# Kernel optimization log

Hardware: AMD Instinct MI355X
Metric: run time of the kernel (lower is better)

## Reference

```python
import jax, jax.numpy as jnp
import numpy as np

BN_EPS = 1e-5
B, G, IN, OUT = 8192, 430, 25, 4  # batch, num small linears, in/out per linear


def _bn(x, gamma, beta):
    # BatchNorm1d in training mode: biased batch statistics over the batch axis
    m = jnp.mean(x, axis=0)
    v = jnp.var(x, axis=0)
    return (x - m) * jax.lax.rsqrt(v + BN_EPS) * gamma + beta


def setup_inputs() -> dict:
    key = jax.random.key(0)
    ks = jax.random.split(key, 20)

    def lin(k, fan_in, fan_out):
        bound = 1.0 / np.sqrt(fan_in)
        kw, kb = jax.random.split(k)
        W = jax.random.uniform(kw, (fan_in, fan_out), jnp.float32, -bound, bound)
        b = jax.random.uniform(kb, (fan_out,), jnp.float32, -bound, bound)
        return W, b

    X = jax.random.normal(ks[0], (B, G, IN), jnp.float32)
    # 430 small linears as one stacked tensor [G, 25, 4]
    bound = 1.0 / np.sqrt(IN)
    Wg = jax.random.uniform(ks[1], (G, IN, OUT), jnp.float32, -bound, bound)
    bg = jax.random.uniform(ks[2], (G, OUT), jnp.float32, -bound, bound)

    W3, b3 = lin(ks[3], 1720, 1024)
    W4, b4 = lin(ks[4], 1024, 512)
    W5, b5 = lin(ks[5], 512, 256)
    W6, b6 = lin(ks[6], 256, 64)
    W7, b7 = lin(ks[7], 64, 32)
    W8, b8 = lin(ks[8], 32, 2)

    g3, be3 = jnp.ones((1024,), jnp.float32), jnp.zeros((1024,), jnp.float32)
    g4, be4 = jnp.ones((512,), jnp.float32), jnp.zeros((512,), jnp.float32)
    g5, be5 = jnp.ones((256,), jnp.float32), jnp.zeros((256,), jnp.float32)

    return dict(X=X, Wg=Wg, bg=bg, W3=W3, b3=b3, g3=g3, be3=be3,
                W4=W4, b4=b4, g4=g4, be4=be4, W5=W5, b5=b5, g5=g5, be5=be5,
                W6=W6, b6=b6, W7=W7, b7=b7, W8=W8, b8=b8)


def reference(X, Wg, bg, W3, b3, g3, be3, W4, b4, g4, be4,
              W5, b5, g5, be5, W6, b6, W7, b7, W8, b8):
    # Fused batched GEMM replacing the 430-iteration Python loop + cats:
    # [B,G,25] x [G,25,4] -> [B,G,4] -> [B,1720]
    h = jnp.einsum('bgi,gio->bgo', X, Wg) + bg
    h = h.reshape(X.shape[0], -1)  # [B, 1720]
    # Dropout layers are identity (deterministic reference); BN uses batch stats
    h = _bn(h @ W3 + b3, g3, be3)
    h = _bn(h @ W4 + b4, g4, be4)
    h = _bn(h @ W5 + b5, g5, be5)
    h = h @ W6 + b6
    h = h @ W7 + b7
    return h @ W8 + b8  # [B, 2]
```

## Files before the change

### kernel.cpp

```cpp
#include <hip/hip_runtime.h>


typedef __attribute__((ext_vector_type(8))) short bfrag;
typedef __attribute__((ext_vector_type(4))) float f32x4v;

__device__ __forceinline__ float4 ld4(const float* p) {
    return *reinterpret_cast<const float4*>(p);
}
__device__ __forceinline__ void st4(float* p, float4 v) {
    *reinterpret_cast<float4*>(p) = v;
}
__device__ __forceinline__ unsigned short f2b(float f) {
    union { float f; unsigned u; } v; v.f = f;
    unsigned r = v.u + 0x7fffu + ((v.u >> 16) & 1u);
    return (unsigned short)(r >> 16);
}
__device__ __forceinline__ float b2f(unsigned short b) {
    union { unsigned u; float f; } v; v.u = (unsigned)b << 16;
    return v.f;
}
__device__ __forceinline__ void async16(unsigned short* lds,
                                        const unsigned short* g) {
    __builtin_amdgcn_global_load_lds(
        (const __attribute__((address_space(1))) void*)g,
        (__attribute__((address_space(3))) void*)lds, 16, 0, 0);
}

__global__ __launch_bounds__(256) void k_grouped(
    const float* __restrict__ X, const float* __restrict__ Wg,
    const float* __restrict__ bg, unsigned short* __restrict__ H0)
{
    __shared__ float Xs[6400];
    const int tid = threadIdx.x;
    const size_t base = (size_t)blockIdx.x * 6400;
    #pragma unroll
    for (int c = 0; c < 25; ++c)
        Xs[c * 256 + tid] = X[base + c * 256 + tid];
    __syncthreads();

    const int idx = blockIdx.x * 256 + tid;
    const int b = idx / 430;
    const int g = idx - b * 430;
    const float* __restrict__ w = Wg + g * 100;
    float4 acc = ld4(bg + g * 4);
    const float* x = &Xs[tid * 25];
    #pragma unroll
    for (int i = 0; i < 25; ++i) {
        const float xi = x[i];
        const float4 wv = ld4(w + i * 4);
        acc.x = fmaf(xi, wv.x, acc.x);
        acc.y = fmaf(xi, wv.y, acc.y);
        acc.z = fmaf(xi, wv.z, acc.z);
        acc.w = fmaf(xi, wv.w, acc.w);
    }
    ushort4 o;
    o.x = f2b(acc.x); o.y = f2b(acc.y); o.z = f2b(acc.z); o.w = f2b(acc.w);
    unsigned short* row = H0 + (size_t)b * 1728;
    *reinterpret_cast<ushort4*>(row + g * 4) = o;
    if (g == 429) {
        const ushort4 z = {0, 0, 0, 0};
        *reinterpret_cast<ushort4*>(row + 1720) = z;
        *reinterpret_cast<ushort4*>(row + 1724) = z;
    }
}

__global__ __launch_bounds__(256) void k_transpose_w(
    const float* __restrict__ W, unsigned short* __restrict__ Wt,
    int K, int N, int Kpad)
{
    __shared__ float t[32][33];
    const int tx = threadIdx.x, ty = threadIdx.y;
    const int k0 = blockIdx.y * 32, n0 = blockIdx.x * 32;
    #pragma unroll
    for (int r = 0; r < 4; ++r) {
        const int k = k0 + ty + r * 8;
        t[ty + r * 8][tx] = (k < K) ? W[(size_t)k * N + n0 + tx] : 0.f;
    }
    __syncthreads();
    #pragma unroll
    for (int r = 0; r < 4; ++r) {
        const int n = n0 + ty + r * 8;
        Wt[(size_t)n * Kpad + k0 + tx] = f2b(t[tx][ty + r * 8]);
    }
}

__global__ __launch_bounds__(256) void k_scale_w(
    const float* __restrict__ W,
    const float* __restrict__ affa, const float* __restrict__ affc,
    unsigned short* __restrict__ Wt, float* __restrict__ bpart,
    int K, int N)
{
    __shared__ float t[32][33];
    __shared__ float red[8][33];
    const int tx = threadIdx.x, ty = threadIdx.y;
    const int k0 = blockIdx.y * 32, n0 = blockIdx.x * 32;
    #pragma unroll
    for (int r = 0; r < 4; ++r)
        t[ty + r * 8][tx] = W[(size_t)(k0 + ty + r * 8) * N + n0 + tx];
    __syncthreads();
    #pragma unroll
    for (int r = 0; r < 4; ++r) {
        const int n = n0 + ty + r * 8;
        Wt[(size_t)n * K + k0 + tx] = f2b(affa[k0 + tx] * t[tx][ty + r * 8]);
    }
    float s = 0.f;
    #pragma unroll
    for (int j = 0; j < 4; ++j) {
        const int kl = ty * 4 + j;
        s = fmaf(affc[k0 + kl], t[kl][tx], s);
    }
    red[ty][tx] = s;
    __syncthreads();
    if (ty == 0) {
        float acc = red[0][tx];
        #pragma unroll
        for (int r = 1; r < 8; ++r) acc += red[r][tx];
        bpart[(size_t)blockIdx.y * N + n0 + tx] = acc;
    }
}

template<bool BPART>
__global__ __launch_bounds__(256) void k_gemm(
    const unsigned short* __restrict__ A,
    const unsigned short* __restrict__ Bt,
    const float* __restrict__ bias,
    const float* __restrict__ bpart, int nbp,
    unsigned short* __restrict__ Y, float* __restrict__ partial,
    int M, int N, int Ka)
{
    __shared__ __align__(16) unsigned short As[128 * 64];
    __shared__ __align__(16) unsigned short Bs[128 * 64];

    const int tid = threadIdx.x;
    const int m0 = blockIdx.y * 128, n0 = blockIdx.x * 128;
    const int lane = tid & 63, wid = tid >> 6;
    const int wm = wid >> 1, wn = wid & 1;
    const int lr = lane & 15, hi = lane >> 4;

    const int srow = wid * 32 + (lane >> 3);
    const int scol = (lane & 7) * 8;
    const unsigned short* Ap = A + (size_t)(m0 + srow) * Ka + scol;
    const unsigned short* Bp = Bt + (size_t)(n0 + srow) * Ka + scol;
    unsigned short* Asd = &As[(wid * 32) * 64];
    unsigned short* Bsd = &Bs[(wid * 32) * 64];

    f32x4v acc[4][4] = {};

    const int Ksteps = Ka >> 6;
    #pragma unroll
    for (int c = 0; c < 4; ++c) {
        async16(Asd + c * 8 * 64, Ap + (size_t)(c * 8) * Ka);
        async16(Bsd + c * 8 * 64, Bp + (size_t)(c * 8) * Ka);
    }

    for (int s = 0; s < Ksteps; ++s) {
        __syncthreads();
        #pragma unroll
        for (int kc = 0; kc < 64; kc += 32) {
            bfrag af[4], bf[4];
            #pragma unroll
            for (int mt = 0; mt < 4; ++mt)
                af[mt] = *reinterpret_cast<const bfrag*>(
                    &As[(wm * 64 + mt * 16 + lr) * 64 + kc + hi * 8]);
            #pragma unroll
            for (int nt = 0; nt < 4; ++nt)
                bf[nt] = *reinterpret_cast<const bfrag*>(
                    &Bs[(wn * 64 + nt * 16 + lr) * 64 + kc + hi * 8]);
            #pragma unroll
            for (int mt = 0; mt < 4; ++mt)
                #pragma unroll
                for (int nt = 0; nt < 4; ++nt)
                    acc[mt][nt] = __builtin_amdgcn_mfma_f32_16x16x32_bf16(
                        af[mt], bf[nt], acc[mt][nt], 0, 0, 0);
        }
        __syncthreads();
        if (s + 1 < Ksteps) {
            const int k0 = (s + 1) << 6;
            #pragma unroll
            for (int c = 0; c < 4; ++c) {
                async16(Asd + c * 8 * 64, Ap + (size_t)(c * 8) * Ka + k0);
                async16(Bsd + c * 8 * 64, Bp + (size_t)(c * 8) * Ka + k0);
            }
        }
    }

    float bcol[4];
    #pragma unroll
    for (int nt = 0; nt < 4; ++nt) {
        const int n = n0 + wn * 64 + nt * 16 + lr;
        float b = bias[n];
        if (BPART)
            for (int t = 0; t < nbp; ++t) b += bpart[(size_t)t * N + n];
        bcol[nt] = b;
    }

    float csum[4] = {0.f, 0.f, 0.f, 0.f}, csq[4] = {0.f, 0.f, 0.f, 0.f};
    #pragma unroll
    for (int mt = 0; mt < 4; ++mt)
        #pragma unroll
        for (int e = 0; e < 4; ++e) {
            const int m = m0 + wm * 64 + mt * 16 + hi * 4 + e;
            #pragma unroll
            for (int nt = 0; nt < 4; ++nt) {
                const float v = acc[mt][nt][e] + bcol[nt];
                Y[(size_t)m * N + n0 + wn * 64 + nt * 16 + lr] = f2b(v);
                csum[nt] += v; csq[nt] += v * v;
            }
        }

    __syncthreads();
    float* redS = (float*)As;
    float* redQ = (float*)Bs;
    const int slot = wm * 4 + hi;
    #pragma unroll
    for (int nt = 0; nt < 4; ++nt) {
        const int c = wn * 64 + nt * 16 + lr;
        redS[slot * 128 + c] = csum[nt];
        redQ[slot * 128 + c] = csq[nt];
    }
    __syncthreads();
    if (tid < 128) {
        float s = 0.f, q = 0.f;
        #pragma unroll
        for (int t = 0; t < 8; ++t) {
            s += redS[t * 128 + tid];
            q += redQ[t * 128 + tid];
        }
        partial[(size_t)blockIdx.y * (2 * N) + n0 + tid] = s;
        partial[(size_t)blockIdx.y * (2 * N) + N + n0 + tid] = q;
    }
}

__global__ __launch_bounds__(256) void k_bn_finalize(
    const float* __restrict__ partial,
    const float* __restrict__ gamma, const float* __restrict__ beta,
    float* __restrict__ affa, float* __restrict__ affc,
    int N, int Mtiles, float invB)
{
    const int c = blockIdx.x * 256 + threadIdx.x;
    if (c >= N) return;
    float S = 0.f, Q = 0.f;
    for (int t = 0; t < Mtiles; ++t) {
        S += partial[(size_t)t * 2 * N + c];
        Q += partial[(size_t)t * 2 * N + N + c];
    }
    const float mean = S * invB;
    const float var = fmaxf(Q * invB - mean * mean, 0.f);
    const float s = rsqrtf(var + 1e-5f);
    const float a = gamma[c] * s;
    affa[c] = a;
    affc[c] = beta[c] - mean * a;
}

__global__ __launch_bounds__(256) void k_tail(
    const unsigned short* __restrict__ Y5,
    const float* __restrict__ a5, const float* __restrict__ c5,
    const float* __restrict__ W6, const float* __restrict__ b6,
    const float* __restrict__ W7, const float* __restrict__ b7,
    const float* __restrict__ W8, const float* __restrict__ b8,
    float* __restrict__ out)
{
    __shared__ float Xs[32][260];
    __shared__ float h6s[32][66];
    __shared__ float h7s[32][34];
    const int tid = threadIdx.x;
    const int row0 = blockIdx.x * 32;

    #pragma unroll
    for (int c = 0; c < 4; ++c) {
        const int id = c * 256 + tid;
        const int r = id >> 5;
        const int k = (id & 31) * 8;
        const ushort4 u0 = *reinterpret_cast<const ushort4*>(
            Y5 + (size_t)(row0 + r) * 256 + k);
        const ushort4 u1 = *reinterpret_cast<const ushort4*>(
            Y5 + (size_t)(row0 + r) * 256 + k + 4);
        const float4 aa0 = ld4(a5 + k),     cc0 = ld4(c5 + k);
        const float4 aa1 = ld4(a5 + k + 4), cc1 = ld4(c5 + k + 4);
        Xs[r][k + 0] = fmaf(b2f(u0.x), aa0.x, cc0.x);
        Xs[r][k + 1] = fmaf(b2f(u0.y), aa0.y, cc0.y);
        Xs[r][k + 2] = fmaf(b2f(u0.z), aa0.z, cc0.z);
        Xs[r][k + 3] = fmaf(b2f(u0.w), aa0.w, cc0.w);
        Xs[r][k + 4] = fmaf(b2f(u1.x), aa1.x, cc1.x);
        Xs[r][k + 5] = fmaf(b2f(u1.y), aa1.y, cc1.y);
        Xs[r][k + 6] = fmaf(b2f(u1.z), aa1.z, cc1.z);
        Xs[r][k + 7] = fmaf(b2f(u1.w), aa1.w, cc1.w);
    }
    __syncthreads();

    {
        const int o = tid & 63;
        const int rg = tid >> 6;
        const float bb = b6[o];
        float acc[8];
        #pragma unroll
        for (int i = 0; i < 8; ++i) acc[i] = bb;
        for (int k = 0; k < 256; ++k) {
            const float w = W6[k * 64 + o];
            #pragma unroll
            for (int i = 0; i < 8; ++i)
                acc[i] = fmaf(Xs[rg * 8 + i][k], w, acc[i]);
        }
        #pragma unroll
        for (int i = 0; i < 8; ++i) h6s[rg * 8 + i][o] = acc[i];
    }
    __syncthreads();

    {
        const int o = tid & 31;
        const int rg = tid >> 5;
        const float bb = b7[o];
        float acc[4];
        #pragma unroll
        for (int i = 0; i < 4; ++i) acc[i] = bb;
        for (int k = 0; k < 64; ++k) {
            const float w = W7[k * 32 + o];
            #pragma unroll
            for (int i = 0; i < 4; ++i)
                acc[i] = fmaf(h6s[rg * 4 + i][k], w, acc[i]);
        }
        #pragma unroll
        for (int i = 0; i < 4; ++i) h7s[rg * 4 + i][o] = acc[i];
    }
    __syncthreads();

    if (tid < 64) {
        const int r = tid >> 1, o = tid & 1;
        float acc = b8[o];
        #pragma unroll
        for (int k = 0; k < 32; ++k)
            acc = fmaf(h7s[r][k], W8[k * 2 + o], acc);
        out[(size_t)(row0 + r) * 2 + o] = acc;
    }
}

extern "C" void kernel_launch(void* const* d_in, const int* in_sizes, int n_in,
                              void* d_out, int out_size, void* d_ws, size_t ws_size,
                              hipStream_t stream)
{
    const float* X   = (const float*)d_in[0];
    const float* Wg  = (const float*)d_in[1];
    const float* bg  = (const float*)d_in[2];
    const float* W3  = (const float*)d_in[3];
    const float* b3  = (const float*)d_in[4];
    const float* g3  = (const float*)d_in[5];
    const float* be3 = (const float*)d_in[6];
    const float* W4  = (const float*)d_in[7];
    const float* b4  = (const float*)d_in[8];
    const float* g4  = (const float*)d_in[9];
    const float* be4 = (const float*)d_in[10];
    const float* W5  = (const float*)d_in[11];
    const float* b5  = (const float*)d_in[12];
    const float* g5  = (const float*)d_in[13];
    const float* be5 = (const float*)d_in[14];
    const float* W6  = (const float*)d_in[15];
    const float* b6  = (const float*)d_in[16];
    const float* W7  = (const float*)d_in[17];
    const float* b7  = (const float*)d_in[18];
    const float* W8  = (const float*)d_in[19];
    const float* b8  = (const float*)d_in[20];
    float* out = (float*)d_out;

    char* wsb = (char*)d_ws;
    unsigned short* H0  = (unsigned short*)wsb;
    unsigned short* Y4  = (unsigned short*)wsb;
    unsigned short* Y3  = (unsigned short*)(wsb + 28311552);
    unsigned short* Y5  = Y3;
    unsigned short* Wt3 = (unsigned short*)(wsb + 45088768);
    unsigned short* Wt4 = (unsigned short*)(wsb + 48627712);
    unsigned short* Wt5 = (unsigned short*)(wsb + 49676288);
    float* partial      = (float*)(wsb + 49938432);
    float* bpart4       = (float*)(wsb + 50462720);
    float* bpart5       = (float*)(wsb + 50528256);
    float* a3 = (float*)(wsb + 50544640);
    float* c3 = a3 + 1024;
    float* a4 = c3 + 1024;
    float* c4 = a4 + 512;
    float* a5 = c4 + 512;
    float* c5 = a5 + 256;

    const float invB = 1.f / 8192.f;

    k_transpose_w<<<dim3(32, 54), dim3(32, 8), 0, stream>>>(W3, Wt3, 1720, 1024, 1728);
    k_grouped<<<13760, 256, 0, stream>>>(X, Wg, bg, H0);

    k_gemm<false><<<dim3(8, 64), 256, 0, stream>>>(
        H0, Wt3, b3, nullptr, 0, Y3, partial, 8192, 1024, 1728);
    k_bn_finalize<<<4, 256, 0, stream>>>(partial, g3, be3, a3, c3, 1024, 64, invB);

    k_scale_w<<<dim3(16, 32), dim3(32, 8), 0, stream>>>(W4, a3, c3, Wt4, bpart4, 1024, 512);
    k_gemm<true><<<dim3(4, 64), 256, 0, stream>>>(
        Y3, Wt4, b4, bpart4, 32, Y4, partial, 8192, 512, 1024);
    k_bn_finalize<<<2, 256, 0, stream>>>(partial, g4, be4, a4, c4, 512, 64, invB);

    k_scale_w<<<dim3(8, 16), dim3(32, 8), 0, stream>>>(W5, a4, c4, Wt5, bpart5, 512, 256);
    k_gemm<true><<<dim3(2, 64), 256, 0, stream>>>(
        Y4, Wt5, b5, bpart5, 16, Y5, partial, 8192, 256, 512);
    k_bn_finalize<<<1, 256, 0, stream>>>(partial, g5, be5, a5, c5, 256, 64, invB);

    k_tail<<<256, 256, 0, stream>>>(Y5, a5, c5, W6, b6, W7, b7, W8, b8, out);
}
```

Before: 366.4 us.

## Tile grouped linear by batch and group blocks with weights staged in LDS

The grouped 430-way small-linear kernel now uses a 2D grid of 32 batch rows by 8 groups per block. Each block loads its 8 groups' weights and biases into shared memory once and reads them from LDS instead of re-reading Wg from global or L1 per thread. Each X row segment is 200 contiguous floats rather than one fully contiguous chunk, so the global loads for X are less coalesced than before. The last group-column block handles the 6-group tail and writes the zero padding.

```diff
diff --git a/kernel.cpp b/kernel.cpp
--- a/kernel.cpp
+++ b/kernel.cpp
@@ -30,37 +30,57 @@
     const float* __restrict__ X, const float* __restrict__ Wg,
     const float* __restrict__ bg, unsigned short* __restrict__ H0)
 {
-    __shared__ float Xs[6400];
+    __shared__ float Xs[32 * 200];
+    __shared__ float Ws[800];
+    __shared__ float Bs[32];
     const int tid = threadIdx.x;
-    const size_t base = (size_t)blockIdx.x * 6400;
-    #pragma unroll
-    for (int c = 0; c < 25; ++c)
-        Xs[c * 256 + tid] = X[base + c * 256 + tid];
-    __syncthreads();
-
-    const int idx = blockIdx.x * 256 + tid;
-    const int b = idx / 430;
-    const int g = idx - b * 430;
-    const float* __restrict__ w = Wg + g * 100;
-    float4 acc = ld4(bg + g * 4);
-    const float* x = &Xs[tid * 25];
-    #pragma unroll
-    for (int i = 0; i < 25; ++i) {
-        const float xi = x[i];
-        const float4 wv = ld4(w + i * 4);
-        acc.x = fmaf(xi, wv.x, acc.x);
-        acc.y = fmaf(xi, wv.y, acc.y);
-        acc.z = fmaf(xi, wv.z, acc.z);
-        acc.w = fmaf(xi, wv.w, acc.w);
-    }
-    ushort4 o;
-    o.x = f2b(acc.x); o.y = f2b(acc.y); o.z = f2b(acc.z); o.w = f2b(acc.w);
-    unsigned short* row = H0 + (size_t)b * 1728;
-    *reinterpret_cast<ushort4*>(row + g * 4) = o;
-    if (g == 429) {
-        const ushort4 z = {0, 0, 0, 0};
-        *reinterpret_cast<ushort4*>(row + 1720) = z;
-        *reinterpret_cast<ushort4*>(row + 1724) = z;
+    const int b0 = blockIdx.x * 32;
+    const int g0 = blockIdx.y * 8;
+    const int ng = (g0 + 8 <= 430) ? 8 : (430 - g0);
+
+    for (int i = tid; i < ng * 100; i += 256)
+        Ws[i] = Wg[g0 * 100 + i];
+    if (tid < ng * 4) Bs[tid] = bg[g0 * 4 + tid];
+
+    if (ng == 8) {
+        #pragma unroll
+        for (int t = 0; t < 25; ++t) {
+            const int i = t * 256 + tid;
+            const int r = i / 200;
+            const int c = i - r * 200;
+            Xs[r * 200 + c] = X[(size_t)(b0 + r) * 10750 + g0 * 25 + c];
+        }
+    } else {
+        for (int i = tid; i < 32 * 150; i += 256) {
+            const int r = i / 150;
+            const int c = i - r * 150;
+            Xs[r * 200 + c] = X[(size_t)(b0 + r) * 10750 + g0 * 25 + c];
+        }
+    }
+    __syncthreads();
+
+    const int bl = tid >> 3, gl = tid & 7;
+    if (gl < ng) {
+        const float* __restrict__ w = &Ws[gl * 100];
+        const float* __restrict__ x = &Xs[bl * 200 + gl * 25];
+        float4 acc = ld4(&Bs[gl * 4]);
+        #pragma unroll
+        for (int i = 0; i < 25; ++i) {
+            const float xi = x[i];
+            const float4 wv = ld4(&w[i * 4]);
+            acc.x = fmaf(xi, wv.x, acc.x);
+            acc.y = fmaf(xi, wv.y, acc.y);
+            acc.z = fmaf(xi, wv.z, acc.z);
+            acc.w = fmaf(xi, wv.w, acc.w);
+        }
+        ushort4 o;
+        o.x = f2b(acc.x); o.y = f2b(acc.y); o.z = f2b(acc.z); o.w = f2b(acc.w);
+        *reinterpret_cast<ushort4*>(
+            H0 + (size_t)(b0 + bl) * 1728 + (size_t)(g0 + gl) * 4) = o;
+    }
+    if (blockIdx.y == 53) {
+        const int r = tid >> 3, c = tid & 7;
+        H0[(size_t)(b0 + r) * 1728 + 1720 + c] = 0;
     }
 }
 
@@ -382,7 +402,7 @@
     const float invB = 1.f / 8192.f;
 
     k_transpose_w<<<dim3(32, 54), dim3(32, 8), 0, stream>>>(W3, Wt3, 1720, 1024, 1728);
-    k_grouped<<<13760, 256, 0, stream>>>(X, Wg, bg, H0);
+    k_grouped<<<dim3(256, 54), 256, 0, stream>>>(X, Wg, bg, H0);
 
     k_gemm<false><<<dim3(8, 64), 256, 0, stream>>>(
         H0, Wt3, b3, nullptr, 0, Y3, partial, 8192, 1024, 1728);
```

Result: faster. 297.0 us (-18.9%).
